# Performance work log

Hardware: AMD Instinct MI355X
Metric: run time of the kernel (lower is better)

## Reference

```python
import jax, jax.numpy as jnp
import numpy as np

NUM_HEADS = 32
NUM_KV_HEADS = 8
HEAD_DIM = 128
SCALE = 0.08838834764831845  # 1/sqrt(128)
NUM_SEQS = 8
BLKS_PER_SEQ = 64
MEM_BLOCK_SIZE = 32          # ctx_len = 64*32 = 2048 per sequence
Q_LEN = 64                   # active diffusion block per sequence
N_BLOCKS = 1024


def setup_inputs() -> dict:
    key = jax.random.key(0)
    k1, k2, k3, k4, k5 = jax.random.split(key, 5)
    T = NUM_SEQS * Q_LEN
    q = jax.random.normal(k1, (T, NUM_HEADS * HEAD_DIM), dtype=jnp.float32)
    k = jax.random.normal(k2, (T, NUM_KV_HEADS * HEAD_DIM), dtype=jnp.float32)
    v = jax.random.normal(k3, (T, NUM_KV_HEADS * HEAD_DIM), dtype=jnp.float32)
    k_cache = jax.random.normal(k4, (N_BLOCKS, MEM_BLOCK_SIZE, NUM_KV_HEADS, HEAD_DIM), dtype=jnp.float32)
    v_cache = jax.random.normal(k5, (N_BLOCKS, MEM_BLOCK_SIZE, NUM_KV_HEADS, HEAD_DIM), dtype=jnp.float32)
    # each sequence owns a distinct contiguous set of cache blocks
    block_tables = jnp.arange(NUM_SEQS * BLKS_PER_SEQ, dtype=jnp.int32).reshape(NUM_SEQS, BLKS_PER_SEQ)
    return {"q": q, "k": k, "v": v, "k_cache": k_cache, "v_cache": v_cache,
            "block_tables": block_tables}


def reference(q, k, v, k_cache, v_cache, block_tables):
    S, B = block_tables.shape
    ctx_len = B * MEM_BLOCK_SIZE
    G = NUM_HEADS // NUM_KV_HEADS  # GQA group size

    # reshape flattened token streams: [T, H*D] -> [S, L, H, D]
    qh = q.reshape(S, Q_LEN, NUM_KV_HEADS, G, HEAD_DIM)
    kn = k.reshape(S, Q_LEN, NUM_KV_HEADS, HEAD_DIM)
    vn = v.reshape(S, Q_LEN, NUM_KV_HEADS, HEAD_DIM)

    # paged gather: block_tables -> [S, B, MEM_BLK, Hkv, D] -> [S, ctx_len, Hkv, D]
    kc = k_cache[block_tables].reshape(S, ctx_len, NUM_KV_HEADS, HEAD_DIM)
    vc = v_cache[block_tables].reshape(S, ctx_len, NUM_KV_HEADS, HEAD_DIM)

    # packed KV = gathered context ++ new active-block tokens (load_kvcache kernel)
    K = jnp.concatenate([kc, kn], axis=1)  # [S, ctx_len+Q_LEN, Hkv, D]
    V = jnp.concatenate([vc, vn], axis=1)

    # diffusion-LM mask: active block attends bidirectionally to full context + itself
    scores = jnp.einsum('sqhgd,skhd->shgqk', qh, K) * SCALE
    probs = jax.nn.softmax(scores, axis=-1)
    out = jnp.einsum('shgqk,skhd->sqhgd', probs, V)
    return out.reshape(S * Q_LEN, NUM_HEADS * HEAD_DIM)
```

## Files before the change

### kernel.cpp

```cpp
#include <hip/hip_runtime.h>

#define NUM_HEADS 32
#define NUM_KV_HEADS 8
#define HEAD_DIM 128
#define GQA 4
#define NUM_SEQS 8
#define BLKS_PER_SEQ 64
#define MEM_BLK 32
#define Q_LEN 64
#define SCALE 0.08838834764831845f

typedef __attribute__((ext_vector_type(4))) float f4;
typedef __attribute__((ext_vector_type(4))) float f32x4;
typedef __attribute__((ext_vector_type(8))) short short8;
typedef __attribute__((ext_vector_type(4))) unsigned int u32x4;

__device__ __forceinline__ unsigned short f2bf(float f) {
  unsigned int u = __builtin_bit_cast(unsigned int, f);
  u += 0x7fffu + ((u >> 16) & 1u);
  return (unsigned short)(u >> 16);
}

#define K_OFF   0
#define V_OFF   16384
#define P_OFF   32768
#define ML_OFF  (32768 + 10240)
#define LDS_BYTES (32768 + 10240 + 512)

__device__ __forceinline__ unsigned k_addr(int key, int d) {
  return (unsigned)(key * 256 + ((d * 2) ^ ((key & 7) << 4)));
}
__device__ __forceinline__ unsigned v_addr(int d, int key) {
  return (unsigned)(d * 64 + ((key * 2) ^ (((d >> 2) & 3) << 4)));
}

__global__ __launch_bounds__(512, 2)
void attn_paged_kernel(const float* __restrict__ q, const float* __restrict__ kn,
                       const float* __restrict__ vn, const float* __restrict__ kc,
                       const float* __restrict__ vc, const int* __restrict__ btab,
                       float* __restrict__ out)
{
  __shared__ __align__(16) char lds[LDS_BYTES];

  const int bid = blockIdx.x;
  const int sh  = bid & 63;
  const int g   = bid >> 6;
  const int s   = sh >> 3;
  const int h   = sh & 7;
  const int tid  = threadIdx.x;
  const int wave = tid >> 6, lane = tid & 63;
  const int rg  = wave & 3;
  const int par = wave >> 2;
  const int lhi = lane >> 4, llo = lane & 15;

  short8 qf[4];
  {
    const float* qrow = q + (size_t)(s * Q_LEN + rg * 16 + llo) * 4096 + (h * GQA + g) * 128;
#pragma unroll
    for (int c = 0; c < 4; ++c) {
      const float* p = qrow + c * 32 + lhi * 8;
      f4 a = *(const f4*)p;
      f4 b = *(const f4*)(p + 4);
      short8 f;
      f[0] = (short)f2bf(a[0]); f[1] = (short)f2bf(a[1]);
      f[2] = (short)f2bf(a[2]); f[3] = (short)f2bf(a[3]);
      f[4] = (short)f2bf(b[0]); f[5] = (short)f2bf(b[1]);
      f[6] = (short)f2bf(b[2]); f[7] = (short)f2bf(b[3]);
      qf[c] = f;
    }
  }

  f32x4 of[8];
#pragma unroll
  for (int i = 0; i < 8; ++i) of[i] = (f32x4){0.f, 0.f, 0.f, 0.f};
  float m_run[4], l_run[4];
#pragma unroll
  for (int r = 0; r < 4; ++r) { m_run[r] = -1e30f; l_run[r] = 0.f; }

  const int ktk = tid >> 4;
  const int kc0 = (tid & 15) * 8;
  const int vcq = tid & 31;
  const int vtp = tid >> 5;

  for (int it = 0; it < 33; ++it) {
#pragma unroll
    for (int pp = 0; pp < 2; ++pp) {
      const int tile = 2 * it + pp;
      const float *ks, *vs0, *vs1;
      if (tile < BLKS_PER_SEQ) {
        const int pb = btab[s * BLKS_PER_SEQ + tile];
        const float* kb_ = kc + ((size_t)pb * MEM_BLK * NUM_KV_HEADS + h) * HEAD_DIM;
        const float* vb_ = vc + ((size_t)pb * MEM_BLK * NUM_KV_HEADS + h) * HEAD_DIM;
        ks  = kb_ + (size_t)ktk * (NUM_KV_HEADS * HEAD_DIM) + kc0;
        vs0 = vb_ + (size_t)(2 * vtp)     * (NUM_KV_HEADS * HEAD_DIM) + vcq * 4;
        vs1 = vb_ + (size_t)(2 * vtp + 1) * (NUM_KV_HEADS * HEAD_DIM) + vcq * 4;
      } else {
        const int base_t = (tile - BLKS_PER_SEQ) * MEM_BLK;
        ks  = kn + (size_t)(s * Q_LEN + base_t + ktk) * 1024 + h * HEAD_DIM + kc0;
        vs0 = vn + (size_t)(s * Q_LEN + base_t + 2 * vtp)     * 1024 + h * HEAD_DIM + vcq * 4;
        vs1 = vn + (size_t)(s * Q_LEN + base_t + 2 * vtp + 1) * 1024 + h * HEAD_DIM + vcq * 4;
      }
      f4 ka = *(const f4*)ks;  f4 kb2 = *(const f4*)(ks + 4);
      f4 va = *(const f4*)vs0; f4 vb2 = *(const f4*)vs1;
      u32x4 pk;
      pk[0] = (unsigned)f2bf(ka[0])  | ((unsigned)f2bf(ka[1])  << 16);
      pk[1] = (unsigned)f2bf(ka[2])  | ((unsigned)f2bf(ka[3])  << 16);
      pk[2] = (unsigned)f2bf(kb2[0]) | ((unsigned)f2bf(kb2[1]) << 16);
      pk[3] = (unsigned)f2bf(kb2[2]) | ((unsigned)f2bf(kb2[3]) << 16);
      *(u32x4*)(lds + K_OFF + pp * 8192 + k_addr(ktk, kc0)) = pk;
#pragma unroll
      for (int i = 0; i < 4; ++i) {
        unsigned w = (unsigned)f2bf(va[i]) | ((unsigned)f2bf(vb2[i]) << 16);
        *(unsigned*)(lds + V_OFF + pp * 8192 + v_addr(vcq * 4 + i, 2 * vtp)) = w;
      }
    }
    __syncthreads();

    {
      const char* kb  = lds + K_OFF + par * 8192;
      const char* vbp = lds + V_OFF + par * 8192;
      f32x4 s0 = {0.f, 0.f, 0.f, 0.f}, s1 = {0.f, 0.f, 0.f, 0.f};
#pragma unroll
      for (int c = 0; c < 4; ++c) {
        short8 kf0 = *(const short8*)(kb + k_addr(llo,      c * 32 + lhi * 8));
        short8 kf1 = *(const short8*)(kb + k_addr(llo + 16, c * 32 + lhi * 8));
        s0 = __builtin_amdgcn_mfma_f32_16x16x32_bf16(qf[c], kf0, s0, 0, 0, 0);
        s1 = __builtin_amdgcn_mfma_f32_16x16x32_bf16(qf[c], kf1, s1, 0, 0, 0);
      }
      float p0[4], p1[4], corr[4], tred[4];
#pragma unroll
      for (int r = 0; r < 4; ++r) {
        s0[r] *= SCALE; s1[r] *= SCALE;
        tred[r] = fmaxf(s0[r], s1[r]);
      }
#pragma unroll
      for (int off = 1; off < 16; off <<= 1)
#pragma unroll
        for (int r = 0; r < 4; ++r) tred[r] = fmaxf(tred[r], __shfl_xor(tred[r], off, 64));
#pragma unroll
      for (int r = 0; r < 4; ++r) {
        float mnew = fmaxf(m_run[r], tred[r]);
        corr[r] = __expf(m_run[r] - mnew);
        p0[r] = __expf(s0[r] - mnew);
        p1[r] = __expf(s1[r] - mnew);
        m_run[r] = mnew;
        tred[r] = p0[r] + p1[r];
      }
#pragma unroll
      for (int off = 1; off < 16; off <<= 1)
#pragma unroll
        for (int r = 0; r < 4; ++r) tred[r] += __shfl_xor(tred[r], off, 64);
#pragma unroll
      for (int r = 0; r < 4; ++r) l_run[r] = l_run[r] * corr[r] + tred[r];
#pragma unroll
      for (int dc = 0; dc < 8; ++dc)
#pragma unroll
        for (int r = 0; r < 4; ++r) of[dc][r] *= corr[r];

      char* pb_ = lds + P_OFF + wave * 1280;
#pragma unroll
      for (int r = 0; r < 4; ++r) {
        const int row = lhi * 4 + r;
        *(unsigned short*)(pb_ + row * 80 + llo * 2)        = f2bf(p0[r]);
        *(unsigned short*)(pb_ + row * 80 + (llo + 16) * 2) = f2bf(p1[r]);
      }
      short8 pa = *(const short8*)(pb_ + llo * 80 + lhi * 16);
#pragma unroll
      for (int dc = 0; dc < 8; ++dc) {
        short8 vf = *(const short8*)(vbp + v_addr(dc * 16 + llo, lhi * 8));
        of[dc] = __builtin_amdgcn_mfma_f32_16x16x32_bf16(pa, vf, of[dc], 0, 0, 0);
      }
    }
    __syncthreads();
  }

  if (par == 1) {
    char* mo = lds + rg * 8192;
#pragma unroll
    for (int dc = 0; dc < 8; ++dc)
#pragma unroll
      for (int r = 0; r < 4; ++r)
        *(float*)(mo + (lhi * 4 + r) * 512 + (dc * 16 + llo) * 4) = of[dc][r];
    if (llo == 0) {
      char* ml = lds + ML_OFF + rg * 128;
#pragma unroll
      for (int r = 0; r < 4; ++r) {
        *(float*)(ml + (lhi * 4 + r) * 8)     = m_run[r];
        *(float*)(ml + (lhi * 4 + r) * 8 + 4) = l_run[r];
      }
    }
  }
  __syncthreads();
  if (par == 0) {
    const char* mo = lds + rg * 8192;
    const char* ml = lds + ML_OFF + rg * 128;
    float ca[4], cb[4], inv[4];
#pragma unroll
    for (int r = 0; r < 4; ++r) {
      const float mb = *(const float*)(ml + (lhi * 4 + r) * 8);
      const float lb = *(const float*)(ml + (lhi * 4 + r) * 8 + 4);
      const float mf = fmaxf(m_run[r], mb);
      ca[r] = __expf(m_run[r] - mf);
      cb[r] = __expf(mb - mf);
      inv[r] = 1.f / (ca[r] * l_run[r] + cb[r] * lb);
    }
#pragma unroll
    for (int dc = 0; dc < 8; ++dc)
#pragma unroll
      for (int r = 0; r < 4; ++r) {
        const float ob = *(const float*)(mo + (lhi * 4 + r) * 512 + (dc * 16 + llo) * 4);
        const float val = (ca[r] * of[dc][r] + cb[r] * ob) * inv[r];
        out[(size_t)(s * Q_LEN + rg * 16 + lhi * 4 + r) * 4096
            + (size_t)((h * GQA + g) * 128 + dc * 16 + llo)] = val;
      }
  }
}

extern "C" void kernel_launch(void* const* d_in, const int* in_sizes, int n_in,
                              void* d_out, int out_size, void* d_ws, size_t ws_size,
                              hipStream_t stream) {
  (void)in_sizes; (void)n_in; (void)d_ws; (void)ws_size; (void)out_size;
  const float* q  = (const float*)d_in[0];
  const float* k  = (const float*)d_in[1];
  const float* v  = (const float*)d_in[2];
  const float* kc = (const float*)d_in[3];
  const float* vc = (const float*)d_in[4];
  const int* bt   = (const int*)d_in[5];
  float* out = (float*)d_out;
  attn_paged_kernel<<<dim3(256), dim3(512), 0, stream>>>(q, k, v, kc, vc, bt, out);
}
```

Measured before the change: 332.1 us.

## Prefetch next KV tiles into registers during compute, with exp2 softmax and lazy rescale

Global loads for the next pair of KV tiles are issued into registers before the current tile's MFMA/softmax work, then converted and written to LDS after a barrier. This hides global memory latency behind compute instead of stalling at the top of each iteration. It also folds scale*log2e into Q so softmax can use exp2, switches to the hardware packed bf16 convert instruction, caches block-table entries in LDS, and skips the output rescale when no row max grows anywhere in the wave. The cost is higher register pressure from the prefetch buffers and an extra barrier per iteration.

```diff
diff --git a/kernel.cpp b/kernel.cpp
--- a/kernel.cpp
+++ b/kernel.cpp
@@ -9,12 +9,18 @@
 #define MEM_BLK 32
 #define Q_LEN 64
 #define SCALE 0.08838834764831845f
+#define RLN2 1.4426950408889634f
 
 typedef __attribute__((ext_vector_type(4))) float f4;
 typedef __attribute__((ext_vector_type(4))) float f32x4;
 typedef __attribute__((ext_vector_type(8))) short short8;
 typedef __attribute__((ext_vector_type(4))) unsigned int u32x4;
 
+__device__ __forceinline__ unsigned cvt_pk(float lo, float hi) {
+  unsigned r;
+  asm("v_cvt_pk_bf16_f32 %0, %1, %2" : "=v"(r) : "v"(lo), "v"(hi));
+  return r;
+}
 __device__ __forceinline__ unsigned short f2bf(float f) {
   unsigned int u = __builtin_bit_cast(unsigned int, f);
   u += 0x7fffu + ((u >> 16) & 1u);
@@ -24,8 +30,9 @@
 #define K_OFF   0
 #define V_OFF   16384
 #define P_OFF   32768
-#define ML_OFF  (32768 + 10240)
-#define LDS_BYTES (32768 + 10240 + 512)
+#define ML_OFF  43008
+#define BT_OFF  43520
+#define LDS_BYTES 43776
 
 __device__ __forceinline__ unsigned k_addr(int key, int d) {
   return (unsigned)(key * 256 + ((d * 2) ^ ((key & 7) << 4)));
@@ -53,20 +60,23 @@
   const int par = wave >> 2;
   const int lhi = lane >> 4, llo = lane & 15;
 
+  if (tid < 64) *(int*)(lds + BT_OFF + tid * 4) = btab[s * BLKS_PER_SEQ + tid];
+
   short8 qf[4];
   {
+    const float qsc = SCALE * RLN2;
     const float* qrow = q + (size_t)(s * Q_LEN + rg * 16 + llo) * 4096 + (h * GQA + g) * 128;
 #pragma unroll
     for (int c = 0; c < 4; ++c) {
       const float* p = qrow + c * 32 + lhi * 8;
       f4 a = *(const f4*)p;
       f4 b = *(const f4*)(p + 4);
-      short8 f;
-      f[0] = (short)f2bf(a[0]); f[1] = (short)f2bf(a[1]);
-      f[2] = (short)f2bf(a[2]); f[3] = (short)f2bf(a[3]);
-      f[4] = (short)f2bf(b[0]); f[5] = (short)f2bf(b[1]);
-      f[6] = (short)f2bf(b[2]); f[7] = (short)f2bf(b[3]);
-      qf[c] = f;
+      u32x4 w;
+      w[0] = cvt_pk(a[0] * qsc, a[1] * qsc);
+      w[1] = cvt_pk(a[2] * qsc, a[3] * qsc);
+      w[2] = cvt_pk(b[0] * qsc, b[1] * qsc);
+      w[3] = cvt_pk(b[2] * qsc, b[3] * qsc);
+      qf[c] = __builtin_bit_cast(short8, w);
     }
   }
 
@@ -81,40 +91,56 @@
   const int kc0 = (tid & 15) * 8;
   const int vcq = tid & 31;
   const int vtp = tid >> 5;
+  const size_t k_toff  = (size_t)ktk * 1024 + h * HEAD_DIM + kc0;
+  const size_t v_toff0 = (size_t)(2 * vtp) * 1024 + h * HEAD_DIM + vcq * 4;
+  char* kw  = lds + K_OFF + k_addr(ktk, kc0);
+  char* vw0 = lds + V_OFF + v_addr(vcq * 4, 2 * vtp);
+
+  __syncthreads();
+
+  f4 rka[2], rkb[2], rva[2], rvb[2];
+
+  auto issue_loads = [&](int it_next) {
+#pragma unroll
+    for (int pp = 0; pp < 2; ++pp) {
+      const int tile = 2 * it_next + pp;
+      const float *kb_, *vb_;
+      if (tile < BLKS_PER_SEQ) {
+        const int pb = *(const int*)(lds + BT_OFF + tile * 4);
+        kb_ = kc + (size_t)pb * 32768;
+        vb_ = vc + (size_t)pb * 32768;
+      } else {
+        const size_t row = (size_t)(s * Q_LEN + (tile - BLKS_PER_SEQ) * MEM_BLK) * 1024;
+        kb_ = kn + row;
+        vb_ = vn + row;
+      }
+      rka[pp] = *(const f4*)(kb_ + k_toff);
+      rkb[pp] = *(const f4*)(kb_ + k_toff + 4);
+      rva[pp] = *(const f4*)(vb_ + v_toff0);
+      rvb[pp] = *(const f4*)(vb_ + v_toff0 + 1024);
+    }
+  };
+  auto write_tiles = [&]() {
+#pragma unroll
+    for (int pp = 0; pp < 2; ++pp) {
+      u32x4 w;
+      w[0] = cvt_pk(rka[pp][0], rka[pp][1]);
+      w[1] = cvt_pk(rka[pp][2], rka[pp][3]);
+      w[2] = cvt_pk(rkb[pp][0], rkb[pp][1]);
+      w[3] = cvt_pk(rkb[pp][2], rkb[pp][3]);
+      *(u32x4*)(kw + pp * 8192) = w;
+#pragma unroll
+      for (int i = 0; i < 4; ++i)
+        *(unsigned*)(vw0 + pp * 8192 + i * 64) = cvt_pk(rva[pp][i], rvb[pp][i]);
+    }
+  };
+
+  issue_loads(0);
+  write_tiles();
+  __syncthreads();
 
   for (int it = 0; it < 33; ++it) {
-#pragma unroll
-    for (int pp = 0; pp < 2; ++pp) {
-      const int tile = 2 * it + pp;
-      const float *ks, *vs0, *vs1;
-      if (tile < BLKS_PER_SEQ) {
-        const int pb = btab[s * BLKS_PER_SEQ + tile];
-        const float* kb_ = kc + ((size_t)pb * MEM_BLK * NUM_KV_HEADS + h) * HEAD_DIM;
-        const float* vb_ = vc + ((size_t)pb * MEM_BLK * NUM_KV_HEADS + h) * HEAD_DIM;
-        ks  = kb_ + (size_t)ktk * (NUM_KV_HEADS * HEAD_DIM) + kc0;
-        vs0 = vb_ + (size_t)(2 * vtp)     * (NUM_KV_HEADS * HEAD_DIM) + vcq * 4;
-        vs1 = vb_ + (size_t)(2 * vtp + 1) * (NUM_KV_HEADS * HEAD_DIM) + vcq * 4;
-      } else {
-        const int base_t = (tile - BLKS_PER_SEQ) * MEM_BLK;
-        ks  = kn + (size_t)(s * Q_LEN + base_t + ktk) * 1024 + h * HEAD_DIM + kc0;
-        vs0 = vn + (size_t)(s * Q_LEN + base_t + 2 * vtp)     * 1024 + h * HEAD_DIM + vcq * 4;
-        vs1 = vn + (size_t)(s * Q_LEN + base_t + 2 * vtp + 1) * 1024 + h * HEAD_DIM + vcq * 4;
-      }
-      f4 ka = *(const f4*)ks;  f4 kb2 = *(const f4*)(ks + 4);
-      f4 va = *(const f4*)vs0; f4 vb2 = *(const f4*)vs1;
-      u32x4 pk;
-      pk[0] = (unsigned)f2bf(ka[0])  | ((unsigned)f2bf(ka[1])  << 16);
-      pk[1] = (unsigned)f2bf(ka[2])  | ((unsigned)f2bf(ka[3])  << 16);
-      pk[2] = (unsigned)f2bf(kb2[0]) | ((unsigned)f2bf(kb2[1]) << 16);
-      pk[3] = (unsigned)f2bf(kb2[2]) | ((unsigned)f2bf(kb2[3]) << 16);
-      *(u32x4*)(lds + K_OFF + pp * 8192 + k_addr(ktk, kc0)) = pk;
-#pragma unroll
-      for (int i = 0; i < 4; ++i) {
-        unsigned w = (unsigned)f2bf(va[i]) | ((unsigned)f2bf(vb2[i]) << 16);
-        *(unsigned*)(lds + V_OFF + pp * 8192 + v_addr(vcq * 4 + i, 2 * vtp)) = w;
-      }
-    }
-    __syncthreads();
+    if (it < 32) issue_loads(it + 1);
 
     {
       const char* kb  = lds + K_OFF + par * 8192;
@@ -127,35 +153,47 @@
         s0 = __builtin_amdgcn_mfma_f32_16x16x32_bf16(qf[c], kf0, s0, 0, 0, 0);
         s1 = __builtin_amdgcn_mfma_f32_16x16x32_bf16(qf[c], kf1, s1, 0, 0, 0);
       }
-      float p0[4], p1[4], corr[4], tred[4];
-#pragma unroll
-      for (int r = 0; r < 4; ++r) {
-        s0[r] *= SCALE; s1[r] *= SCALE;
-        tred[r] = fmaxf(s0[r], s1[r]);
-      }
+      float p0[4], p1[4], tred[4];
+#pragma unroll
+      for (int r = 0; r < 4; ++r) tred[r] = fmaxf(s0[r], s1[r]);
 #pragma unroll
       for (int off = 1; off < 16; off <<= 1)
 #pragma unroll
         for (int r = 0; r < 4; ++r) tred[r] = fmaxf(tred[r], __shfl_xor(tred[r], off, 64));
-#pragma unroll
-      for (int r = 0; r < 4; ++r) {
-        float mnew = fmaxf(m_run[r], tred[r]);
-        corr[r] = __expf(m_run[r] - mnew);
-        p0[r] = __expf(s0[r] - mnew);
-        p1[r] = __expf(s1[r] - mnew);
-        m_run[r] = mnew;
+
+      bool grow = (tred[0] > m_run[0]) | (tred[1] > m_run[1]) |
+                  (tred[2] > m_run[2]) | (tred[3] > m_run[3]);
+      const int resc = __any((int)grow);
+      float corr[4];
+      if (resc) {
+#pragma unroll
+        for (int r = 0; r < 4; ++r) {
+          const float mnew = fmaxf(m_run[r], tred[r]);
+          corr[r] = exp2f(m_run[r] - mnew);
+          m_run[r] = mnew;
+        }
+      }
+#pragma unroll
+      for (int r = 0; r < 4; ++r) {
+        p0[r] = exp2f(s0[r] - m_run[r]);
+        p1[r] = exp2f(s1[r] - m_run[r]);
         tred[r] = p0[r] + p1[r];
       }
 #pragma unroll
       for (int off = 1; off < 16; off <<= 1)
 #pragma unroll
         for (int r = 0; r < 4; ++r) tred[r] += __shfl_xor(tred[r], off, 64);
-#pragma unroll
-      for (int r = 0; r < 4; ++r) l_run[r] = l_run[r] * corr[r] + tred[r];
-#pragma unroll
-      for (int dc = 0; dc < 8; ++dc)
-#pragma unroll
-        for (int r = 0; r < 4; ++r) of[dc][r] *= corr[r];
+      if (resc) {
+#pragma unroll
+        for (int r = 0; r < 4; ++r) l_run[r] = l_run[r] * corr[r] + tred[r];
+#pragma unroll
+        for (int dc = 0; dc < 8; ++dc)
+#pragma unroll
+          for (int r = 0; r < 4; ++r) of[dc][r] *= corr[r];
+      } else {
+#pragma unroll
+        for (int r = 0; r < 4; ++r) l_run[r] += tred[r];
+      }
 
       char* pb_ = lds + P_OFF + wave * 1280;
 #pragma unroll
@@ -171,6 +209,9 @@
         of[dc] = __builtin_amdgcn_mfma_f32_16x16x32_bf16(pa, vf, of[dc], 0, 0, 0);
       }
     }
+
+    __syncthreads();
+    if (it < 32) write_tiles();
     __syncthreads();
   }
 
@@ -200,8 +241,8 @@
       const float mb = *(const float*)(ml + (lhi * 4 + r) * 8);
       const float lb = *(const float*)(ml + (lhi * 4 + r) * 8 + 4);
       const float mf = fmaxf(m_run[r], mb);
-      ca[r] = __expf(m_run[r] - mf);
-      cb[r] = __expf(mb - mf);
+      ca[r] = exp2f(m_run[r] - mf);
+      cb[r] = exp2f(mb - mf);
       inv[r] = 1.f / (ca[r] * l_run[r] + cb[r] * lb);
     }
 #pragma unroll
```

After: 300.8 us. 9.4% less time.
